# Optimization experiments

Measured on AMD Instinct MI355X. Metric: run time of the kernel, lower is better.

## Reference

```python
import jax, jax.numpy as jnp
import numpy as np
from jax import lax

B, T1, T2, D, H = 4, 1024, 1024, 1024, 16
DK = D // H          # 64 per-head dim
K = 13               # conv kernel size
FF = 4 * D


def _ln(x, g, b, eps):
    mu = jnp.mean(x, axis=-1, keepdims=True)
    var = jnp.mean((x - mu) ** 2, axis=-1, keepdims=True)
    y = (x - mu) * lax.rsqrt(var + eps)
    if g is not None:
        y = y * g + b
    return y


def _conv1d(x, w, b):
    # x: (B, T, C) ; w: (O, C//H, K) grouped conv, 'same' padding
    y = lax.conv_general_dilated(
        x.transpose(0, 2, 1), w, window_strides=(1,),
        padding=[(K // 2, K // 2)],
        dimension_numbers=('NCH', 'OIH', 'NCH'),
        feature_group_count=H)
    return (y + b[None, :, None]).transpose(0, 2, 1)


def setup_inputs() -> dict:
    key = jax.random.key(0)
    ks = jax.random.split(key, 24)
    s = 0.02
    inp = {
        'noisy_feats': jax.random.normal(ks[0], (B, T1, D), jnp.float32),
        'clean_feats': jax.random.normal(ks[1], (B, T2, D), jnp.float32),
        't': jax.random.normal(ks[2], (B, D), jnp.float32),
        'ln_noisy_g': jnp.ones((D,), jnp.float32),
        'ln_noisy_b': jnp.zeros((D,), jnp.float32),
        'ln_clean_g': jnp.ones((D,), jnp.float32),
        'ln_clean_b': jnp.zeros((D,), jnp.float32),
        'ada_w': jax.random.normal(ks[3], (6 * D, D), jnp.float32) * s,
        'ada_b': jnp.zeros((6 * D,), jnp.float32),
        'wq': jax.random.normal(ks[4], (D, D // H, K), jnp.float32) * s,
        'bq': jnp.zeros((D,), jnp.float32),
        'wk': jax.random.normal(ks[5], (D, D // H, K), jnp.float32) * s,
        'bk': jnp.zeros((D,), jnp.float32),
        'wv': jax.random.normal(ks[6], (D, D // H, K), jnp.float32) * s,
        'bv': jnp.zeros((D,), jnp.float32),
        'fc_w': jax.random.normal(ks[7], (D, D), jnp.float32) * s,
        'fc_b': jnp.zeros((D,), jnp.float32),
        'ff_w1': jax.random.normal(ks[8], (FF, D), jnp.float32) * s,
        'ff_b1': jnp.zeros((FF,), jnp.float32),
        'ff_w2': jax.random.normal(ks[9], (D, FF), jnp.float32) * s,
        'ff_b2': jnp.zeros((D,), jnp.float32),
        'noisy_lengths': jax.random.randint(ks[10], (B,), 1, T1 + 1),
        'clean_lengths': jax.random.randint(ks[11], (B,), 1, T2 + 1),
    }
    return inp


def reference(noisy_feats, clean_feats, t,
              ln_noisy_g, ln_noisy_b, ln_clean_g, ln_clean_b,
              ada_w, ada_b, wq, bq, wk, bk, wv, bv, fc_w, fc_b,
              ff_w1, ff_b1, ff_w2, ff_b2,
              noisy_lengths, clean_lengths):
    # pre-norms (affine, eps=1e-5 torch default)
    noisy = _ln(noisy_feats, ln_noisy_g, ln_noisy_b, 1e-5)
    clean = _ln(clean_feats, ln_clean_g, ln_clean_b, 1e-5)

    # AdaLayerNormZero
    emb = jax.nn.silu(t) @ ada_w.T + ada_b                      # (B, 6D)
    shift_msa, scale_msa, gate_msa, shift_mlp, scale_mlp, gate_mlp = jnp.split(emb, 6, axis=1)
    normx = _ln(noisy, None, None, 1e-6) * (1.0 + scale_msa[:, None]) + shift_msa[:, None]

    # padding mask: True at pad positions (only context mask enters the scores)
    clean_mask = jnp.arange(T2)[None, :] >= clean_lengths[:, None]   # (B, T2)

    # grouped-conv QKV
    q = _conv1d(normx, wq, bq).reshape(B, T1, H, DK)
    k = _conv1d(clean, wk, bk).reshape(B, T2, H, DK)
    v = _conv1d(clean, wv, bv).reshape(B, T2, H, DK)

    scores = jnp.einsum('bqhd,bkhd->bhqk', q, k) / jnp.sqrt(jnp.float32(DK))
    scores = jnp.where(clean_mask[:, None, None, :], jnp.float32(-1e30), scores)
    p = jax.nn.softmax(scores, axis=-1)
    # rows where every key is masked -> zero (torch all_inf handling)
    all_masked = jnp.all(clean_mask, axis=-1)[:, None, None, None]
    p = jnp.where(all_masked, 0.0, p)

    out = jnp.einsum('bhqk,bkhd->bqhd', p, v).reshape(B, T1, D)
    out = out @ fc_w.T + fc_b

    x = noisy + gate_msa[:, None, :] * out
    n2 = _ln(x, None, None, 1e-6) * (1.0 + scale_mlp[:, None]) + shift_mlp[:, None]
    ff = jax.nn.gelu(n2 @ ff_w1.T + ff_b1, approximate=True) @ ff_w2.T + ff_b2
    return x + gate_mlp[:, None, :] * ff
```

## Files before the change

kernel.cpp:

```cpp
#include <hip/hip_runtime.h>
#include <hip/hip_bf16.h>

typedef __hip_bfloat16 bf16;
typedef __attribute__((ext_vector_type(8))) short short8;
typedef __attribute__((ext_vector_type(4))) float f32x4;

#define D_ 1024
#define SIXD 6144

__device__ __forceinline__ float bflo(unsigned int u){ union {unsigned int u; float f;} c; c.u = u << 16; return c.f; }
__device__ __forceinline__ float bfhi(unsigned int u){ union {unsigned int u; float f;} c; c.u = u & 0xFFFF0000u; return c.f; }
__device__ __forceinline__ float bload(const bf16* p){
  union {unsigned int u; float f;} c;
  c.u = ((unsigned int)(*reinterpret_cast<const unsigned short*>(p))) << 16;
  return c.f;
}
__device__ __forceinline__ bf16 bstore(float f){ return __float2bfloat16(f); }

__device__ __forceinline__ void gload16(const bf16* g, bf16* l){
  __builtin_amdgcn_global_load_lds((const __attribute__((address_space(1))) unsigned int*)g,
                                   (__attribute__((address_space(3))) unsigned int*)l, 16, 0, 0);
}

__device__ __forceinline__ void pipe_sync(){
  asm volatile("s_waitcnt vmcnt(0)" ::: "memory");
  __builtin_amdgcn_s_barrier();
  __builtin_amdgcn_sched_barrier(0);
}

template<int ISBF>
__device__ __forceinline__ float ild(const void* p, size_t i){
  if (ISBF) return bload((const bf16*)p + i);
  return ((const float*)p)[i];
}

__device__ __forceinline__ float block_sum(float v, float* sh4){
  #pragma unroll
  for (int o = 32; o; o >>= 1) v += __shfl_down(v, o);
  __syncthreads();
  int lane = threadIdx.x & 63, wid = threadIdx.x >> 6;
  if (lane == 0) sh4[wid] = v;
  __syncthreads();
  return sh4[0] + sh4[1] + sh4[2] + sh4[3];
}

__global__ void detect_kernel(const unsigned int* g, int* flag){
  unsigned int u = *g;
  *flag = (u == 0x3F803F80u) ? 1 : 0;
}

template<int ISBF>
__device__ __forceinline__ void emb_body(const void* T, const void* AW, const void* AB,
                                         float* E, float* st){
  int b = blockIdx.y;
  int tid = threadIdx.x;
  for (int c = tid; c < D_; c += 256) {
    float x = ild<ISBF>(T, (size_t)b*D_ + c);
    st[c] = x / (1.f + expf(-x));
  }
  __syncthreads();
  int wid = tid >> 6, lane = tid & 63;
  int j = blockIdx.x * 4 + wid;
  float dot = 0.f;
  for (int c = lane; c < D_; c += 64) dot += ild<ISBF>(AW, (size_t)j*D_ + c) * st[c];
  #pragma unroll
  for (int o = 32; o; o >>= 1) dot += __shfl_down(dot, o);
  if (lane == 0) E[b*SIXD + j] = dot + ild<ISBF>(AB, j);
}
__global__ __launch_bounds__(256) void emb_kernel(const void* T, const void* AW, const void* AB,
                                                  const int* flagp, float* E){
  __shared__ float st[D_];
  if (*flagp) emb_body<1>(T, AW, AB, E, st); else emb_body<0>(T, AW, AB, E, st);
}

template<int ISBF>
__device__ __forceinline__ void ln_noisy_body(const void* X, const void* G, const void* Bt,
                                              const float* E, bf16* xbuf, bf16* normx, float* sh4){
  int r = blockIdx.x; int b = r >> 10;
  int tid = threadIdx.x; int c0 = tid * 4;
  size_t base = (size_t)r*D_ + c0;
  float f0 = ild<ISBF>(X, base+0), f1 = ild<ISBF>(X, base+1);
  float f2 = ild<ISBF>(X, base+2), f3 = ild<ISBF>(X, base+3);
  float mean = block_sum(f0+f1+f2+f3, sh4) * (1.f/D_);
  float var  = block_sum(f0*f0+f1*f1+f2*f2+f3*f3, sh4) * (1.f/D_) - mean*mean;
  float rstd = rsqrtf(fmaxf(var, 0.f) + 1e-5f);
  float y0 = (f0-mean)*rstd*ild<ISBF>(G,c0+0) + ild<ISBF>(Bt,c0+0);
  float y1 = (f1-mean)*rstd*ild<ISBF>(G,c0+1) + ild<ISBF>(Bt,c0+1);
  float y2 = (f2-mean)*rstd*ild<ISBF>(G,c0+2) + ild<ISBF>(Bt,c0+2);
  float y3 = (f3-mean)*rstd*ild<ISBF>(G,c0+3) + ild<ISBF>(Bt,c0+3);
  bf16* xo = xbuf + base;
  xo[0]=bstore(y0); xo[1]=bstore(y1); xo[2]=bstore(y2); xo[3]=bstore(y3);
  float m2 = block_sum(y0+y1+y2+y3, sh4) * (1.f/D_);
  float v2 = block_sum(y0*y0+y1*y1+y2*y2+y3*y3, sh4) * (1.f/D_) - m2*m2;
  float rstd2 = rsqrtf(fmaxf(v2, 0.f) + 1e-6f);
  const float* eb = E + b*SIXD;
  bf16* o = normx + base;
  o[0] = bstore((y0-m2)*rstd2*(1.f+eb[1024+c0+0]) + eb[c0+0]);
  o[1] = bstore((y1-m2)*rstd2*(1.f+eb[1024+c0+1]) + eb[c0+1]);
  o[2] = bstore((y2-m2)*rstd2*(1.f+eb[1024+c0+2]) + eb[c0+2]);
  o[3] = bstore((y3-m2)*rstd2*(1.f+eb[1024+c0+3]) + eb[c0+3]);
}
__global__ __launch_bounds__(256) void ln_noisy_fused(const void* X, const void* G, const void* Bt,
                                                      const float* E, bf16* xbuf, bf16* normx,
                                                      const int* flagp){
  __shared__ float sh4[4];
  if (*flagp) ln_noisy_body<1>(X,G,Bt,E,xbuf,normx,sh4); else ln_noisy_body<0>(X,G,Bt,E,xbuf,normx,sh4);
}

template<int ISBF>
__device__ __forceinline__ void ln_clean_body(const void* X, const void* G, const void* Bt,
                                              bf16* Y, float* sh4){
  int r = blockIdx.x;
  int tid = threadIdx.x; int c0 = tid * 4;
  size_t base = (size_t)r*D_ + c0;
  float f0 = ild<ISBF>(X, base+0), f1 = ild<ISBF>(X, base+1);
  float f2 = ild<ISBF>(X, base+2), f3 = ild<ISBF>(X, base+3);
  float mean = block_sum(f0+f1+f2+f3, sh4) * (1.f/D_);
  float var  = block_sum(f0*f0+f1*f1+f2*f2+f3*f3, sh4) * (1.f/D_) - mean*mean;
  float rstd = rsqrtf(fmaxf(var, 0.f) + 1e-5f);
  bf16* o = Y + base;
  o[0] = bstore((f0-mean)*rstd*ild<ISBF>(G,c0+0) + ild<ISBF>(Bt,c0+0));
  o[1] = bstore((f1-mean)*rstd*ild<ISBF>(G,c0+1) + ild<ISBF>(Bt,c0+1));
  o[2] = bstore((f2-mean)*rstd*ild<ISBF>(G,c0+2) + ild<ISBF>(Bt,c0+2));
  o[3] = bstore((f3-mean)*rstd*ild<ISBF>(G,c0+3) + ild<ISBF>(Bt,c0+3));
}
__global__ __launch_bounds__(256) void ln_clean_kernel(const void* X, const void* G, const void* Bt,
                                                       bf16* Y, const int* flagp){
  __shared__ float sh4[4];
  if (*flagp) ln_clean_body<1>(X,G,Bt,Y,sh4); else ln_clean_body<0>(X,G,Bt,Y,sh4);
}

__global__ __launch_bounds__(256) void ln2_kernel(const bf16* __restrict__ X, const float* __restrict__ E,
                                                  bf16* __restrict__ Y){
  __shared__ float sh4[4];
  int r = blockIdx.x; int b = r >> 10;
  int tid = threadIdx.x; int c0 = tid * 4;
  uint2 u = *reinterpret_cast<const uint2*>(X + (size_t)r*D_ + c0);
  float f0 = bflo(u.x), f1 = bfhi(u.x), f2 = bflo(u.y), f3 = bfhi(u.y);
  float mean = block_sum(f0+f1+f2+f3, sh4) * (1.f/D_);
  float var  = block_sum(f0*f0+f1*f1+f2*f2+f3*f3, sh4) * (1.f/D_) - mean*mean;
  float rstd = rsqrtf(fmaxf(var, 0.f) + 1e-6f);
  const float* eb = E + b*SIXD;
  bf16* o = Y + (size_t)r*D_ + c0;
  o[0] = bstore((f0-mean)*rstd*(1.f+eb[4096+c0+0]) + eb[3072+c0+0]);
  o[1] = bstore((f1-mean)*rstd*(1.f+eb[4096+c0+1]) + eb[3072+c0+1]);
  o[2] = bstore((f2-mean)*rstd*(1.f+eb[4096+c0+2]) + eb[3072+c0+2]);
  o[3] = bstore((f3-mean)*rstd*(1.f+eb[4096+c0+3]) + eb[3072+c0+3]);
}

template<int ISBF>
__device__ __forceinline__ void wtrans_body(const void* W, bf16* Wtr){
  size_t idx = (size_t)blockIdx.x * 256 + threadIdx.x;
  int si = idx & 63;
  size_t r = idx >> 6;
  int o = (int)(r & 63); r >>= 6;
  int k = (int)(r % 13);
  int g = (int)(r / 13);
  int i = si ^ ((o & 7) << 3);
  Wtr[idx] = bstore(ild<ISBF>(W, ((size_t)(g*64 + o)*64 + i)*13 + k));
}
__global__ __launch_bounds__(256) void conv_wtrans(const void* W, bf16* Wtr, const int* flagp){
  if (*flagp) wtrans_body<1>(W, Wtr); else wtrans_body<0>(W, Wtr);
}

template<int ISBF>
__device__ __forceinline__ void wconv_body(const void* W, bf16* o, int n){
  for (int i = blockIdx.x*256 + threadIdx.x; i < n; i += gridDim.x*256)
    o[i] = bstore(ild<ISBF>(W, (size_t)i));
}
__global__ __launch_bounds__(256) void wconv_kernel(const void* W, bf16* o, int n, const int* flagp){
  if (*flagp) wconv_body<1>(W, o, n); else wconv_body<0>(W, o, n);
}

template<int ISBF>
__device__ __forceinline__ void convl_body(const bf16* __restrict__ X,
                                           const bf16* __restrict__ Wtr, const void* Bias,
                                           bf16* __restrict__ Y,
                                           bf16* ws, bf16* xs){
  int tid = threadIdx.x;
  int wave = tid >> 6, lane = tid & 63;
  int fr = lane & 15, fq = lane >> 4;
  int t0 = blockIdx.x * 256;
  int g = blockIdx.y, b = blockIdx.z;
  const bf16* Wg = Wtr + (size_t)g*53248;
  #pragma unroll
  for (int p = 0; p < 13; ++p)
    gload16(Wg + ((size_t)p*512 + tid)*8, ws + (p*512 + tid)*8);
  const bf16* xg = X + ((size_t)b*1024)*D_ + g*64;
  for (int idx = tid; idx < 268*8; idx += 512) {
    int row = idx >> 3, q = idx & 7;
    int t = t0 - 6 + row;
    uint4 v = make_uint4(0,0,0,0);
    if (t >= 0 && t < 1024)
      v = *reinterpret_cast<const uint4*>(xg + (size_t)t*D_ + q*8);
    *reinterpret_cast<uint4*>(&xs[row*72 + q*8]) = v;
  }
  __syncthreads();
  f32x4 acc[2][4];
  #pragma unroll
  for (int i = 0; i < 2; ++i)
    #pragma unroll
    for (int j = 0; j < 4; ++j) acc[i][j] = (f32x4){0.f,0.f,0.f,0.f};
  int wrow = wave * 32;
  const bf16* a0 = xs + (wrow + fr)*72 + fq*8;
  for (int k = 0; k < 13; ++k) {
    const bf16* wk_ = ws + (k*64 + fr)*64;
    const bf16* ar = a0 + k*72;
    #pragma unroll
    for (int h = 0; h < 2; ++h) {
      int swz = (h*32 + fq*8) ^ ((fr & 7) << 3);
      short8 af0 = *reinterpret_cast<const short8*>(ar + h*32);
      short8 af1 = *reinterpret_cast<const short8*>(ar + 16*72 + h*32);
      #pragma unroll
      for (int tn = 0; tn < 4; ++tn) {
        short8 bv = *reinterpret_cast<const short8*>(wk_ + tn*1024 + swz);
        acc[0][tn] = __builtin_amdgcn_mfma_f32_16x16x32_bf16(af0, bv, acc[0][tn], 0,0,0);
        acc[1][tn] = __builtin_amdgcn_mfma_f32_16x16x32_bf16(af1, bv, acc[1][tn], 0,0,0);
      }
    }
  }
  #pragma unroll
  for (int tm = 0; tm < 2; ++tm) {
    #pragma unroll
    for (int tn = 0; tn < 4; ++tn) {
      int oc = g*64 + tn*16 + fr;
      float bb = ild<ISBF>(Bias, oc);
      #pragma unroll
      for (int r = 0; r < 4; ++r) {
        int tt = t0 + wrow + tm*16 + fq*4 + r;
        Y[((size_t)(b*1024 + tt))*D_ + oc] = bstore(acc[tm][tn][r] + bb);
      }
    }
  }
}
__global__ __launch_bounds__(512) void conv_lds(const bf16* X, const bf16* Wtr, const void* Bias,
                                                bf16* Y, const int* flagp){
  extern __shared__ bf16 smem[];
  bf16* ws = smem;
  bf16* xs = smem + 53248;
  if (*flagp) convl_body<1>(X, Wtr, Bias, Y, ws, xs);
  else        convl_body<0>(X, Wtr, Bias, Y, ws, xs);
}
#define CONV_LDS_BYTES ((53248 + 268*72) * 2)

__global__ __launch_bounds__(256) void attn_mfma(const bf16* __restrict__ Q, const bf16* __restrict__ Kb,
                                                 const bf16* __restrict__ V, const int* __restrict__ lens,
                                                 bf16* __restrict__ O){
  __shared__ bf16 qs[64*72];
  __shared__ bf16 ks[32*72];
  __shared__ bf16 vt[64*40];
  __shared__ bf16 ps[4][16*40];
  int tid = threadIdx.x;
  int wave = tid >> 6, lane = tid & 63;
  int fr = lane & 15, fq = lane >> 4;
  int qb = blockIdx.x, h = blockIdx.y, b = blockIdx.z;
  int len = lens[b]; len = len < 0 ? 0 : (len > 1024 ? 1024 : len);
  {
    int row = tid >> 2, col = (tid & 3) * 16;
    const bf16* src = Q + ((size_t)(b*1024 + qb*64 + row))*D_ + h*64 + col;
    *reinterpret_cast<uint4*>(&qs[row*72 + col])     = *reinterpret_cast<const uint4*>(src);
    *reinterpret_cast<uint4*>(&qs[row*72 + col + 8]) = *reinterpret_cast<const uint4*>(src + 8);
  }
  f32x4 oacc[4];
  #pragma unroll
  for (int t = 0; t < 4; ++t) oacc[t] = (f32x4){0.f,0.f,0.f,0.f};
  float mrow[4] = {-1e30f,-1e30f,-1e30f,-1e30f};
  float lrow[4] = {0.f,0.f,0.f,0.f};
  int srow = tid >> 3, scol = (tid & 7) * 8;
  const bf16* kg = Kb + ((size_t)b*1024)*D_ + h*64;
  const bf16* vg = V  + ((size_t)b*1024)*D_ + h*64;
  const bf16* aptr = &qs[(wave*16 + fr)*72 + fq*8];
  for (int k0 = 0; k0 < len; k0 += 32) {
    int kr = k0 + srow;
    uint4 kv = make_uint4(0,0,0,0), vv = make_uint4(0,0,0,0);
    if (kr < len) {
      kv = *reinterpret_cast<const uint4*>(kg + (size_t)kr*D_ + scol);
      vv = *reinterpret_cast<const uint4*>(vg + (size_t)kr*D_ + scol);
    }
    __syncthreads();
    *reinterpret_cast<uint4*>(&ks[srow*72 + scol]) = kv;
    {
      union { uint4 u; unsigned short s[8]; } c; c.u = vv;
      #pragma unroll
      for (int j = 0; j < 8; ++j)
        *reinterpret_cast<unsigned short*>(&vt[(scol+j)*40 + srow]) = c.s[j];
    }
    __syncthreads();
    short8 aq0 = *reinterpret_cast<const short8*>(aptr);
    short8 aq1 = *reinterpret_cast<const short8*>(aptr + 32);
    f32x4 s0 = (f32x4){0.f,0.f,0.f,0.f}, s1 = (f32x4){0.f,0.f,0.f,0.f};
    s0 = __builtin_amdgcn_mfma_f32_16x16x32_bf16(aq0, *reinterpret_cast<const short8*>(&ks[fr*72 + fq*8]), s0, 0,0,0);
    s0 = __builtin_amdgcn_mfma_f32_16x16x32_bf16(aq1, *reinterpret_cast<const short8*>(&ks[fr*72 + 32 + fq*8]), s0, 0,0,0);
    s1 = __builtin_amdgcn_mfma_f32_16x16x32_bf16(aq0, *reinterpret_cast<const short8*>(&ks[(16+fr)*72 + fq*8]), s1, 0,0,0);
    s1 = __builtin_amdgcn_mfma_f32_16x16x32_bf16(aq1, *reinterpret_cast<const short8*>(&ks[(16+fr)*72 + 32 + fq*8]), s1, 0,0,0);
    bool v0 = (k0 + fr) < len;
    bool v1 = (k0 + 16 + fr) < len;
    #pragma unroll
    for (int r = 0; r < 4; ++r) {
      float sv0 = v0 ? s0[r]*0.125f : -1e30f;
      float sv1 = v1 ? s1[r]*0.125f : -1e30f;
      float rmax = fmaxf(sv0, sv1);
      rmax = fmaxf(rmax, __shfl_xor(rmax, 1));
      rmax = fmaxf(rmax, __shfl_xor(rmax, 2));
      rmax = fmaxf(rmax, __shfl_xor(rmax, 4));
      rmax = fmaxf(rmax, __shfl_xor(rmax, 8));
      float mnew = fmaxf(mrow[r], rmax);
      float alpha = __expf(mrow[r] - mnew);
      float p0 = __expf(sv0 - mnew);
      float p1 = __expf(sv1 - mnew);
      float psum = p0 + p1;
      psum += __shfl_xor(psum, 1);
      psum += __shfl_xor(psum, 2);
      psum += __shfl_xor(psum, 4);
      psum += __shfl_xor(psum, 8);
      lrow[r] = lrow[r]*alpha + psum;
      mrow[r] = mnew;
      ps[wave][(fq*4+r)*40 + fr]      = bstore(p0);
      ps[wave][(fq*4+r)*40 + 16 + fr] = bstore(p1);
      oacc[0][r] *= alpha; oacc[1][r] *= alpha;
      oacc[2][r] *= alpha; oacc[3][r] *= alpha;
    }
    short8 ap = *reinterpret_cast<const short8*>(&ps[wave][fr*40 + fq*8]);
    #pragma unroll
    for (int tn = 0; tn < 4; ++tn) {
      short8 bv = *reinterpret_cast<const short8*>(&vt[(tn*16+fr)*40 + fq*8]);
      oacc[tn] = __builtin_amdgcn_mfma_f32_16x16x32_bf16(ap, bv, oacc[tn], 0,0,0);
    }
  }
  #pragma unroll
  for (int r = 0; r < 4; ++r) {
    float inv = (lrow[r] > 0.f) ? 1.f/lrow[r] : 0.f;
    int q = qb*64 + wave*16 + fq*4 + r;
    bf16* op = O + ((size_t)(b*1024 + q))*D_ + h*64 + fr;
    #pragma unroll
    for (int tn = 0; tn < 4; ++tn)
      op[tn*16] = bstore(oacc[tn][r] * inv);
  }
}

template<int ISBF>
__device__ __forceinline__ void mgemm_body(const bf16* __restrict__ A, const bf16* __restrict__ W,
                                           const void* bias, int bofs,
                                           int K, int ldA, int ldW, int Nst, int mode, int gate_ofs,
                                           bf16* xbuf, const float* emb, void* outb,
                                           bf16* As, bf16* Bs){
  int tid = threadIdx.x;
  int m0 = blockIdx.y * 128, n0 = blockIdx.x * 128;
  int wave = tid >> 6, lane = tid & 63;
  int wr = wave >> 2, wc = wave & 3;
  int fr = lane & 15, fq = lane >> 4;
  int srow = tid >> 2, skc = (tid & 3) * 8;
  const bf16* Ag = A + (size_t)(m0 + srow)*ldA + skc;
  const bf16* Wg = W + (size_t)(n0 + srow)*ldW + skc;
  bf16* Asl = As + tid*8;
  bf16* Bsl = Bs + tid*8;
  const bf16* Afr = As + (wr*64 + fr)*32 + fq*8;
  const bf16* Bfr = Bs + (wc*32 + fr)*32 + fq*8;
  f32x4 acc[4][2];
  #pragma unroll
  for (int i = 0; i < 4; ++i)
    #pragma unroll
    for (int j = 0; j < 2; ++j) acc[i][j] = (f32x4){0.f,0.f,0.f,0.f};
  gload16(Ag,      Asl);
  gload16(Ag + 32, Asl + 4096);
  gload16(Wg,      Bsl);
  gload16(Wg + 32, Bsl + 4096);
  pipe_sync();
  int cur = 0;
  int nt = K >> 6;
  for (int t = 0; t < nt; ++t) {
    if (t + 1 < nt) {
      int k1 = (t + 1) << 6;
      int bo = (cur ^ 1) * 8192;
      gload16(Ag + k1,      Asl + bo);
      gload16(Ag + k1 + 32, Asl + bo + 4096);
      gload16(Wg + k1,      Bsl + bo);
      gload16(Wg + k1 + 32, Bsl + bo + 4096);
    }
    int co = cur * 8192;
    #pragma unroll
    for (int ks = 0; ks < 2; ++ks) {
      short8 af[4], bfv[2];
      #pragma unroll
      for (int tm = 0; tm < 4; ++tm) af[tm] = *reinterpret_cast<const short8*>(Afr + co + ks*4096 + tm*16*32);
      #pragma unroll
      for (int tn = 0; tn < 2; ++tn) bfv[tn] = *reinterpret_cast<const short8*>(Bfr + co + ks*4096 + tn*16*32);
      #pragma unroll
      for (int tm = 0; tm < 4; ++tm)
        #pragma unroll
        for (int tn = 0; tn < 2; ++tn)
          acc[tm][tn] = __builtin_amdgcn_mfma_f32_16x16x32_bf16(af[tm], bfv[tn], acc[tm][tn], 0, 0, 0);
    }
    if (t + 1 < nt) pipe_sync();
    cur ^= 1;
  }
  #pragma unroll
  for (int tm = 0; tm < 4; ++tm) {
    #pragma unroll
    for (int tn = 0; tn < 2; ++tn) {
      int nn = n0 + wc*32 + tn*16 + fr;
      float bv = bias ? ild<ISBF>(bias, (size_t)(bofs + nn)) : 0.f;
      #pragma unroll
      for (int r = 0; r < 4; ++r) {
        int mm = m0 + wr*64 + tm*16 + fq*4 + r;
        float v = acc[tm][tn][r] + bv;
        const float* eb = emb + (mm >> 10)*SIXD;
        if (mode == 1) {
          float tt = 0.7978845608028654f * (v + 0.044715f * v * v * v);
          ((bf16*)outb)[(size_t)mm*Nst + nn] = bstore(0.5f * v * (1.f + tanhf(tt)));
        } else if (mode == 2) {
          size_t xi = (size_t)mm*1024 + nn;
          xbuf[xi] = bstore(bload(xbuf + xi) + eb[gate_ofs + nn] * v);
        } else {
          size_t xi = (size_t)mm*1024 + nn;
          float rr = bload(xbuf + xi) + eb[gate_ofs + nn] * v;
          if (ISBF) ((bf16*)outb)[xi] = bstore(rr);
          else      ((float*)outb)[xi] = rr;
        }
      }
    }
  }
}
__global__ __launch_bounds__(512) void mgemm_kernel(const bf16* A, const bf16* W,
                                                    const void* bias, int bofs,
                                                    int K, int ldA, int ldW, int Nst, int mode, int gate_ofs,
                                                    bf16* xbuf, const float* emb, void* outb,
                                                    const int* flagp){
  __shared__ bf16 As[2*2*128*32];
  __shared__ bf16 Bs[2*2*128*32];
  if (*flagp) mgemm_body<1>(A,W,bias,bofs,K,ldA,ldW,Nst,mode,gate_ofs,xbuf,emb,outb,As,Bs);
  else        mgemm_body<0>(A,W,bias,bofs,K,ldA,ldW,Nst,mode,gate_ofs,xbuf,emb,outb,As,Bs);
}

extern "C" void kernel_launch(void* const* d_in, const int* in_sizes, int n_in,
                              void* d_out, int out_size, void* d_ws, size_t ws_size,
                              hipStream_t stream) {
  (void)in_sizes; (void)n_in; (void)out_size; (void)ws_size;
  const void* noisy = d_in[0];
  const void* clean = d_in[1];
  const void* t     = d_in[2];
  const void* lng   = d_in[3];
  const void* lnb   = d_in[4];
  const void* lcg   = d_in[5];
  const void* lcb   = d_in[6];
  const void* ada_w = d_in[7];
  const void* ada_b = d_in[8];
  const void* wq    = d_in[9];
  const void* bq    = d_in[10];
  const void* wk    = d_in[11];
  const void* bk    = d_in[12];
  const void* wv    = d_in[13];
  const void* bv    = d_in[14];
  const void* fc_w  = d_in[15];
  const void* fc_b  = d_in[16];
  const void* ff_w1 = d_in[17];
  const void* ff_b1 = d_in[18];
  const void* ff_w2 = d_in[19];
  const void* ff_b2 = d_in[20];
  const int*  clen  = (const int*)d_in[22];

  char* w = (char*)d_ws;
  int*   flagp = (int*)w;
  float* embp  = (float*)(w + 4096);
  bf16*  xbuf  = (bf16*)(w + 102400);
  bf16*  normx = (bf16*)(w + 8491008);
  bf16*  cleanb= (bf16*)(w + 16879616);
  bf16*  qb    = (bf16*)(w + 25268224);
  bf16*  kbuf  = (bf16*)(w + 33656832);
  bf16*  vbuf  = (bf16*)(w + 42045440);
  bf16*  wqtr  = (bf16*)(w + 50434048);
  bf16*  wktr  = (bf16*)(w + 52137984);
  bf16*  wvtr  = (bf16*)(w + 53841920);
  bf16*  ff1h  = qb;
  bf16*  attno = cleanb;
  bf16*  n2b   = normx;
  bf16*  fc_wb = wqtr;
  bf16*  ffw1b = vbuf;
  bf16*  ffw2b = cleanb;

  detect_kernel<<<1, 1, 0, stream>>>((const unsigned int*)lng, flagp);
  emb_kernel<<<dim3(1536, 4), 256, 0, stream>>>(t, ada_w, ada_b, flagp, embp);
  ln_noisy_fused<<<4096, 256, 0, stream>>>(noisy, lng, lnb, embp, xbuf, normx, flagp);
  ln_clean_kernel<<<4096, 256, 0, stream>>>(clean, lcg, lcb, cleanb, flagp);
  conv_wtrans<<<3328, 256, 0, stream>>>(wq, wqtr, flagp);
  conv_wtrans<<<3328, 256, 0, stream>>>(wk, wktr, flagp);
  conv_wtrans<<<3328, 256, 0, stream>>>(wv, wvtr, flagp);
  conv_lds<<<dim3(4, 16, 4), 512, CONV_LDS_BYTES, stream>>>(normx,  wqtr, bq, qb,   flagp);
  conv_lds<<<dim3(4, 16, 4), 512, CONV_LDS_BYTES, stream>>>(cleanb, wktr, bk, kbuf, flagp);
  conv_lds<<<dim3(4, 16, 4), 512, CONV_LDS_BYTES, stream>>>(cleanb, wvtr, bv, vbuf, flagp);
  wconv_kernel<<<1024, 256, 0, stream>>>(fc_w, fc_wb, 1048576, flagp);
  attn_mfma<<<dim3(16, 16, 4), 256, 0, stream>>>(qb, kbuf, vbuf, clen, attno);
  wconv_kernel<<<2048, 256, 0, stream>>>(ff_w1, ffw1b, 4194304, flagp);
  mgemm_kernel<<<dim3(8, 32), 512, 0, stream>>>(attno, fc_wb, fc_b, 0,
                                                1024, 1024, 1024, 1024, 2, 2048, xbuf, embp, nullptr, flagp);
  wconv_kernel<<<2048, 256, 0, stream>>>(ff_w2, ffw2b, 4194304, flagp);
  ln2_kernel<<<4096, 256, 0, stream>>>(xbuf, embp, n2b);
  mgemm_kernel<<<dim3(16, 32), 512, 0, stream>>>(n2b, ffw1b, ff_b1, 0,
                                                 1024, 1024, 1024, 2048, 1, 0, xbuf, embp, ff1h, flagp);
  mgemm_kernel<<<dim3(8, 32), 512, 0, stream>>>(ff1h, ffw2b, ff_b2, 0,
                                                2048, 2048, 4096, 1024, 2, 5120, xbuf, embp, nullptr, flagp);
  mgemm_kernel<<<dim3(16, 32), 512, 0, stream>>>(n2b, ffw1b + (size_t)2048*1024, ff_b1, 2048,
                                                 1024, 1024, 1024, 2048, 1, 0, xbuf, embp, ff1h, flagp);
  mgemm_kernel<<<dim3(8, 32), 512, 0, stream>>>(ff1h, ffw2b + 2048, nullptr, 0,
                                                2048, 2048, 4096, 1024, 3, 5120, xbuf, embp, d_out, flagp);
}
```

Before: 498.4 us.

## Restructure attention kernel: 64-key tiles, transposed S=K·Q, swizzled V LDS layout

The attention kernel now processes 64 keys per iteration instead of 32 and computes scores as K×Q so each lane owns one query column. The row max and sum then need only two cross-lane shuffles instead of four per row. Q fragments are hoisted into registers, and V is written transposed into LDS as packed key pairs with an XOR swizzle to reduce bank conflicts. P is packed into 32-bit stores. This halves the loop trip count and barrier count and cuts per-iteration shuffle work, at the cost of more LDS and registers per block.

After: 474.3 us. 1.05x faster.

```diff
diff --git a/kernel.cpp b/kernel.cpp
--- a/kernel.cpp
+++ b/kernel.cpp
@@ -16,6 +16,10 @@
   return c.f;
 }
 __device__ __forceinline__ bf16 bstore(float f){ return __float2bfloat16(f); }
+__device__ __forceinline__ unsigned short bf16bits(float f){
+  bf16 b = __float2bfloat16(f);
+  return *reinterpret_cast<unsigned short*>(&b);
+}
 
 __device__ __forceinline__ void gload16(const bf16* g, bf16* l){
   __builtin_amdgcn_global_load_lds((const __attribute__((address_space(1))) unsigned int*)g,
@@ -247,9 +251,9 @@
                                                  const bf16* __restrict__ V, const int* __restrict__ lens,
                                                  bf16* __restrict__ O){
   __shared__ bf16 qs[64*72];
-  __shared__ bf16 ks[32*72];
-  __shared__ bf16 vt[64*40];
-  __shared__ bf16 ps[4][16*40];
+  __shared__ bf16 ks[64*72];
+  __shared__ bf16 vt[64*72];
+  __shared__ bf16 ps[4][16*72];
   int tid = threadIdx.x;
   int wave = tid >> 6, lane = tid & 63;
   int fr = lane & 15, fq = lane >> 4;
@@ -261,80 +265,113 @@
     *reinterpret_cast<uint4*>(&qs[row*72 + col])     = *reinterpret_cast<const uint4*>(src);
     *reinterpret_cast<uint4*>(&qs[row*72 + col + 8]) = *reinterpret_cast<const uint4*>(src + 8);
   }
+  __syncthreads();
+  short8 bq0 = *reinterpret_cast<const short8*>(&qs[(wave*16 + fr)*72 + fq*8]);
+  short8 bq1 = *reinterpret_cast<const short8*>(&qs[(wave*16 + fr)*72 + 32 + fq*8]);
   f32x4 oacc[4];
   #pragma unroll
   for (int t = 0; t < 4; ++t) oacc[t] = (f32x4){0.f,0.f,0.f,0.f};
-  float mrow[4] = {-1e30f,-1e30f,-1e30f,-1e30f};
-  float lrow[4] = {0.f,0.f,0.f,0.f};
-  int srow = tid >> 3, scol = (tid & 7) * 8;
+  float m_ = -1e30f, l_ = 0.f;
+  int krow = tid >> 2, kcol = (tid & 3) * 16;
+  int vk = (tid >> 3) * 2, vcol = (tid & 7) * 8;
   const bf16* kg = Kb + ((size_t)b*1024)*D_ + h*64;
   const bf16* vg = V  + ((size_t)b*1024)*D_ + h*64;
-  const bf16* aptr = &qs[(wave*16 + fr)*72 + fq*8];
-  for (int k0 = 0; k0 < len; k0 += 32) {
-    int kr = k0 + srow;
-    uint4 kv = make_uint4(0,0,0,0), vv = make_uint4(0,0,0,0);
-    if (kr < len) {
-      kv = *reinterpret_cast<const uint4*>(kg + (size_t)kr*D_ + scol);
-      vv = *reinterpret_cast<const uint4*>(vg + (size_t)kr*D_ + scol);
-    }
+  for (int k0 = 0; k0 < len; k0 += 64) {
+    uint4 kv0 = make_uint4(0,0,0,0), kv1 = make_uint4(0,0,0,0);
+    uint4 va = make_uint4(0,0,0,0), vb = make_uint4(0,0,0,0);
+    if (k0 + krow < len) {
+      kv0 = *reinterpret_cast<const uint4*>(kg + (size_t)(k0+krow)*D_ + kcol);
+      kv1 = *reinterpret_cast<const uint4*>(kg + (size_t)(k0+krow)*D_ + kcol + 8);
+    }
+    if (k0 + vk < len)     va = *reinterpret_cast<const uint4*>(vg + (size_t)(k0+vk)*D_ + vcol);
+    if (k0 + vk + 1 < len) vb = *reinterpret_cast<const uint4*>(vg + (size_t)(k0+vk+1)*D_ + vcol);
     __syncthreads();
-    *reinterpret_cast<uint4*>(&ks[srow*72 + scol]) = kv;
+    *reinterpret_cast<uint4*>(&ks[krow*72 + kcol])     = kv0;
+    *reinterpret_cast<uint4*>(&ks[krow*72 + kcol + 8]) = kv1;
     {
-      union { uint4 u; unsigned short s[8]; } c; c.u = vv;
-      #pragma unroll
-      for (int j = 0; j < 8; ++j)
-        *reinterpret_cast<unsigned short*>(&vt[(scol+j)*40 + srow]) = c.s[j];
+      union { uint4 u; unsigned short s[8]; } ca, cb; ca.u = va; cb.u = vb;
+      #pragma unroll
+      for (int j = 0; j < 8; ++j) {
+        unsigned int w = ((unsigned int)cb.s[j] << 16) | (unsigned int)ca.s[j];
+        int d = vcol + j;
+        int blk = ((vk >> 3) ^ ((d >> 3) & 7)) << 3;
+        *reinterpret_cast<unsigned int*>(&vt[d*72 + blk + (vk & 7)]) = w;
+      }
     }
     __syncthreads();
-    short8 aq0 = *reinterpret_cast<const short8*>(aptr);
-    short8 aq1 = *reinterpret_cast<const short8*>(aptr + 32);
-    f32x4 s0 = (f32x4){0.f,0.f,0.f,0.f}, s1 = (f32x4){0.f,0.f,0.f,0.f};
-    s0 = __builtin_amdgcn_mfma_f32_16x16x32_bf16(aq0, *reinterpret_cast<const short8*>(&ks[fr*72 + fq*8]), s0, 0,0,0);
-    s0 = __builtin_amdgcn_mfma_f32_16x16x32_bf16(aq1, *reinterpret_cast<const short8*>(&ks[fr*72 + 32 + fq*8]), s0, 0,0,0);
-    s1 = __builtin_amdgcn_mfma_f32_16x16x32_bf16(aq0, *reinterpret_cast<const short8*>(&ks[(16+fr)*72 + fq*8]), s1, 0,0,0);
-    s1 = __builtin_amdgcn_mfma_f32_16x16x32_bf16(aq1, *reinterpret_cast<const short8*>(&ks[(16+fr)*72 + 32 + fq*8]), s1, 0,0,0);
-    bool v0 = (k0 + fr) < len;
-    bool v1 = (k0 + 16 + fr) < len;
-    #pragma unroll
-    for (int r = 0; r < 4; ++r) {
-      float sv0 = v0 ? s0[r]*0.125f : -1e30f;
-      float sv1 = v1 ? s1[r]*0.125f : -1e30f;
-      float rmax = fmaxf(sv0, sv1);
-      rmax = fmaxf(rmax, __shfl_xor(rmax, 1));
-      rmax = fmaxf(rmax, __shfl_xor(rmax, 2));
-      rmax = fmaxf(rmax, __shfl_xor(rmax, 4));
-      rmax = fmaxf(rmax, __shfl_xor(rmax, 8));
-      float mnew = fmaxf(mrow[r], rmax);
-      float alpha = __expf(mrow[r] - mnew);
-      float p0 = __expf(sv0 - mnew);
-      float p1 = __expf(sv1 - mnew);
-      float psum = p0 + p1;
-      psum += __shfl_xor(psum, 1);
-      psum += __shfl_xor(psum, 2);
-      psum += __shfl_xor(psum, 4);
-      psum += __shfl_xor(psum, 8);
-      lrow[r] = lrow[r]*alpha + psum;
-      mrow[r] = mnew;
-      ps[wave][(fq*4+r)*40 + fr]      = bstore(p0);
-      ps[wave][(fq*4+r)*40 + 16 + fr] = bstore(p1);
-      oacc[0][r] *= alpha; oacc[1][r] *= alpha;
-      oacc[2][r] *= alpha; oacc[3][r] *= alpha;
-    }
-    short8 ap = *reinterpret_cast<const short8*>(&ps[wave][fr*40 + fq*8]);
+    f32x4 s[4];
+    #pragma unroll
+    for (int f = 0; f < 4; ++f) {
+      short8 ak0 = *reinterpret_cast<const short8*>(&ks[(f*16 + fr)*72 + fq*8]);
+      short8 ak1 = *reinterpret_cast<const short8*>(&ks[(f*16 + fr)*72 + 32 + fq*8]);
+      s[f] = (f32x4){0.f,0.f,0.f,0.f};
+      s[f] = __builtin_amdgcn_mfma_f32_16x16x32_bf16(ak0, bq0, s[f], 0,0,0);
+      s[f] = __builtin_amdgcn_mfma_f32_16x16x32_bf16(ak1, bq1, s[f], 0,0,0);
+    }
+    float p[4][4];
+    float pmax = -1e30f;
+    #pragma unroll
+    for (int f = 0; f < 4; ++f)
+      #pragma unroll
+      for (int r = 0; r < 4; ++r) {
+        float sv = (k0 + f*16 + fq*4 + r < len) ? s[f][r]*0.125f : -1e30f;
+        p[f][r] = sv;
+        pmax = fmaxf(pmax, sv);
+      }
+    pmax = fmaxf(pmax, __shfl_xor(pmax, 16));
+    pmax = fmaxf(pmax, __shfl_xor(pmax, 32));
+    float mnew = fmaxf(m_, pmax);
+    float alpha = __expf(m_ - mnew);
+    float psum = 0.f;
+    #pragma unroll
+    for (int f = 0; f < 4; ++f)
+      #pragma unroll
+      for (int r = 0; r < 4; ++r) {
+        float pv = __expf(p[f][r] - mnew);
+        p[f][r] = pv;
+        psum += pv;
+      }
+    psum += __shfl_xor(psum, 16);
+    psum += __shfl_xor(psum, 32);
+    l_ = l_*alpha + psum;
+    m_ = mnew;
+    #pragma unroll
+    for (int f = 0; f < 4; ++f) {
+      unsigned int lo = ((unsigned int)bf16bits(p[f][1]) << 16) | (unsigned int)bf16bits(p[f][0]);
+      unsigned int hi = ((unsigned int)bf16bits(p[f][3]) << 16) | (unsigned int)bf16bits(p[f][2]);
+      unsigned int* pp = reinterpret_cast<unsigned int*>(&ps[wave][fr*72 + f*16 + fq*4]);
+      pp[0] = lo; pp[1] = hi;
+    }
+    float aq[4];
+    #pragma unroll
+    for (int r = 0; r < 4; ++r) aq[r] = __shfl(alpha, fq*4 + r);
+    #pragma unroll
+    for (int tn = 0; tn < 4; ++tn)
+      #pragma unroll
+      for (int r = 0; r < 4; ++r) oacc[tn][r] *= aq[r];
+    short8 ap0 = *reinterpret_cast<const short8*>(&ps[wave][fr*72 + fq*8]);
+    short8 ap1 = *reinterpret_cast<const short8*>(&ps[wave][fr*72 + 32 + fq*8]);
     #pragma unroll
     for (int tn = 0; tn < 4; ++tn) {
-      short8 bv = *reinterpret_cast<const short8*>(&vt[(tn*16+fr)*40 + fq*8]);
-      oacc[tn] = __builtin_amdgcn_mfma_f32_16x16x32_bf16(ap, bv, oacc[tn], 0,0,0);
-    }
-  }
+      int d = tn*16 + fr;
+      int sw = (d >> 3) & 7;
+      short8 bv0 = *reinterpret_cast<const short8*>(&vt[d*72 + ((fq     ^ sw) << 3)]);
+      short8 bv1 = *reinterpret_cast<const short8*>(&vt[d*72 + (((4+fq) ^ sw) << 3)]);
+      oacc[tn] = __builtin_amdgcn_mfma_f32_16x16x32_bf16(ap0, bv0, oacc[tn], 0,0,0);
+      oacc[tn] = __builtin_amdgcn_mfma_f32_16x16x32_bf16(ap1, bv1, oacc[tn], 0,0,0);
+    }
+  }
+  float linv = (l_ > 0.f) ? 1.f/l_ : 0.f;
+  float iq[4];
+  #pragma unroll
+  for (int r = 0; r < 4; ++r) iq[r] = __shfl(linv, fq*4 + r);
   #pragma unroll
   for (int r = 0; r < 4; ++r) {
-    float inv = (lrow[r] > 0.f) ? 1.f/lrow[r] : 0.f;
     int q = qb*64 + wave*16 + fq*4 + r;
     bf16* op = O + ((size_t)(b*1024 + q))*D_ + h*64 + fr;
     #pragma unroll
     for (int tn = 0; tn < 4; ++tn)
-      op[tn*16] = bstore(oacc[tn][r] * inv);
+      op[tn*16] = bstore(oacc[tn][r] * iq[r]);
   }
 }
 
```
